# Kernel optimization log

Measured on AMD Instinct MI355X. Metric: run time of the kernel, lower is better.

Reference implementation:

```python
import jax, jax.numpy as jnp
import numpy as np

V = 50257      # vocab_size
EMB = 300      # emb_size
H = 512        # mcan_flat_out_size (GRU hidden)
HS = 256       # hidden_size (object proposal feature dim)
BH = 256       # bi_hidden_size (encoder output feature dim)
NP = 256       # num_proposal
ML = 50        # max_length (lang seq len)
AL = 20        # answer length -> 19 decode steps
NEG = -1e9


def setup_inputs() -> dict:
    key = jax.random.key(0)
    ks = jax.random.split(key, 30)
    s = 0.02
    n = lambda k, sh: (s * jax.random.normal(k, sh)).astype(jnp.float32)
    d = {}
    d["input_tok"] = jax.random.randint(ks[0], (1,), 0, V, dtype=jnp.int32)
    d["hidden"] = jax.random.normal(ks[1], (1, 1, H), jnp.float32)
    d["encoder_outputs"] = jax.random.normal(ks[2], (ML, BH), jnp.float32)
    d["object_proposals"] = jax.random.normal(ks[3], (NP, HS), jnp.float32)
    d["object_mask"] = jax.random.randint(ks[4], (1, NP), 0, 2, dtype=jnp.int32)
    d["lang_mask"] = jax.random.randint(ks[5], (1, ML), 0, 2, dtype=jnp.int32)
    d["answer_to_vocab"] = jax.random.randint(ks[6], (AL,), 0, V, dtype=jnp.int32)
    # learned params (dropout treated as eval/identity)
    d["emb"] = n(ks[7], (V, EMB))
    cin = H + EMB  # 812
    d["attn_w1"] = n(ks[8], (256, cin)); d["attn_b1"] = jnp.zeros((256,), jnp.float32)
    d["attn_w2"] = n(ks[9], (ML, 256)); d["attn_b2"] = jnp.zeros((ML,), jnp.float32)
    d["attn_op_w1"] = n(ks[10], (256, cin)); d["attn_op_b1"] = jnp.zeros((256,), jnp.float32)
    d["attn_op_w2"] = n(ks[11], (NP, 256)); d["attn_op_b2"] = jnp.zeros((NP,), jnp.float32)
    comb_in = HS + BH + EMB  # 812
    d["cmb_w1"] = n(ks[12], (512, comb_in)); d["cmb_b1"] = jnp.zeros((512,), jnp.float32)
    d["cmb_w2"] = n(ks[13], (H, 512)); d["cmb_b2"] = jnp.zeros((H,), jnp.float32)
    d["gru_w_ih"] = n(ks[14], (3 * H, H)); d["gru_w_hh"] = n(ks[15], (3 * H, H))
    d["gru_b_ih"] = jnp.zeros((3 * H,), jnp.float32); d["gru_b_hh"] = jnp.zeros((3 * H,), jnp.float32)
    d["out_w"] = n(ks[16], (V, H)); d["out_b"] = jnp.zeros((V,), jnp.float32)
    return d


def reference(input_tok, hidden, encoder_outputs, object_proposals, object_mask,
              lang_mask, answer_to_vocab, emb, attn_w1, attn_b1, attn_w2, attn_b2,
              attn_op_w1, attn_op_b1, attn_op_w2, attn_op_b2, cmb_w1, cmb_b1,
              cmb_w2, cmb_b2, gru_w_ih, gru_w_hh, gru_b_ih, gru_b_hh, out_w, out_b):
    obj_m = object_mask.astype(bool)   # [1, NP]
    lang_m = lang_mask.astype(bool)    # [1, ML]
    # teacher forcing: step i embeds answer_to_vocab[i] (step 0 uses input_tok)
    tokens = jnp.concatenate([input_tok, answer_to_vocab[1:-1]])  # [AL-1]

    def step(h, tok):
        # h: [1,1,H]
        x = jax.nn.relu(emb[tok])[None, :]                     # [1,EMB]
        cat = jnp.concatenate([x, h[0]], axis=1)               # [1, EMB+H]
        # object attention
        a_op = jax.nn.relu(cat @ attn_op_w1.T + attn_op_b1) @ attn_op_w2.T + attn_op_b2
        a_op = jax.nn.softmax(jnp.where(obj_m, NEG, a_op), axis=1)   # [1,NP]
        ctx_op = a_op @ object_proposals                       # [1,HS]
        # language attention
        a_l = jax.nn.relu(cat @ attn_w1.T + attn_b1) @ attn_w2.T + attn_b2
        a_l = jax.nn.softmax(jnp.where(lang_m, NEG, a_l), axis=1)    # [1,ML]
        ctx = a_l @ encoder_outputs                            # [1,BH]
        comb = jnp.concatenate([x, ctx, ctx_op], axis=1)       # [1, EMB+BH+HS]
        g = jax.nn.relu(jax.nn.relu(comb @ cmb_w1.T + cmb_b1) @ cmb_w2.T + cmb_b2)  # [1,H]
        # GRU cell (torch gate order: r, z, n)
        gi = g @ gru_w_ih.T + gru_b_ih
        gh = h[0] @ gru_w_hh.T + gru_b_hh
        i_r, i_z, i_n = jnp.split(gi, 3, axis=1)
        h_r, h_z, h_n = jnp.split(gh, 3, axis=1)
        r = jax.nn.sigmoid(i_r + h_r)
        z = jax.nn.sigmoid(i_z + h_z)
        nn_ = jnp.tanh(i_n + r * h_n)
        h_new = (1.0 - z) * nn_ + z * h[0]                     # [1,H]
        logits = h_new @ out_w.T + out_b                       # [1,V]
        return h_new[None], (logits, a_l, a_op)

    _, (logits, attn_w, attn_ob_w) = jax.lax.scan(step, hidden, tokens)
    # logits: [AL-1,1,V]; attn_w: [AL-1,1,ML]; attn_ob_w: [AL-1,1,NP]
    return logits, attn_w, attn_ob_w
```

## Files before the change

### kernel.cpp

```cpp
#include <hip/hip_runtime.h>
#include <math.h>

#define T_STEPS 19
#define V 50257
#define EMB 300
#define HDIM 512
#define NP 256
#define ML 50
#define CIN 812
#define NEGV -1e9f
#define NBLK 128

#define OFF_X      0
#define OFF_POP    5700
#define OFF_PL     10564
#define OFF_PC     15428
#define OFF_HS     25156
#define OFF_H1OP   35396
#define OFF_H1L    35652
#define OFF_C1     37444
#define OFF_G      37956
#define OFF_LOGOP  38468
#define OFF_LOGL   38724
#define OFF_MPROP  38788
#define OFF_MENC   169860
#define OFF_BAR    195460

#define OUT_LOGITS 0
#define OUT_ATTW   ((long)T_STEPS * V)
#define OUT_ATTOB  (OUT_ATTW + (long)T_STEPS * ML)

__device__ __forceinline__ float wred(float v) {
  v += __shfl_xor(v, 32, 64);
  v += __shfl_xor(v, 16, 64);
  v += __shfl_xor(v, 8, 64);
  v += __shfl_xor(v, 4, 64);
  v += __shfl_xor(v, 2, 64);
  v += __shfl_xor(v, 1, 64);
  return v;
}

__device__ __forceinline__ float dot4(float4 a, float4 b) {
  return a.x * b.x + a.y * b.y + a.z * b.z + a.w * b.w;
}

__device__ __forceinline__ void gstore(float* p, float v) {
  __hip_atomic_store(p, v, __ATOMIC_RELAXED, __HIP_MEMORY_SCOPE_AGENT);
}
__device__ __forceinline__ float ld1c(const float* p) {
  return __hip_atomic_load(p, __ATOMIC_RELAXED, __HIP_MEMORY_SCOPE_AGENT);
}
__device__ __forceinline__ float2 ld2c(const float* p) {
  unsigned long long u = __hip_atomic_load((const unsigned long long*)p,
                                           __ATOMIC_RELAXED, __HIP_MEMORY_SCOPE_AGENT);
  float2 r;
  r.x = __uint_as_float((unsigned)u);
  r.y = __uint_as_float((unsigned)(u >> 32));
  return r;
}
__device__ __forceinline__ float4 ld4c(const float* p) {
  float2 a = ld2c(p), b = ld2c(p + 2);
  return make_float4(a.x, a.y, b.x, b.y);
}

__device__ __forceinline__ void gbar(float* wsb, unsigned bar) {
  asm volatile("s_waitcnt vmcnt(0)" ::: "memory");
  __syncthreads();
  unsigned* base = (unsigned*)(wsb + OFF_BAR);
  if (threadIdx.x == 0) {
    __hip_atomic_store(base + 16 + 16 * blockIdx.x, bar, __ATOMIC_RELAXED, __HIP_MEMORY_SCOPE_AGENT);
  }
  if (blockIdx.x == 0 && threadIdx.x < 64) {
    unsigned* fa = base + 16 + 32 * threadIdx.x;
    unsigned* fb = fa + 16;
    while (__hip_atomic_load(fa, __ATOMIC_RELAXED, __HIP_MEMORY_SCOPE_AGENT) < bar ||
           __hip_atomic_load(fb, __ATOMIC_RELAXED, __HIP_MEMORY_SCOPE_AGENT) < bar) {
      __builtin_amdgcn_s_sleep(1);
    }
    if (threadIdx.x == 0) {
      __hip_atomic_store(base, bar, __ATOMIC_RELAXED, __HIP_MEMORY_SCOPE_AGENT);
    }
  } else if (threadIdx.x == 0) {
    while (__hip_atomic_load(base, __ATOMIC_RELAXED, __HIP_MEMORY_SCOPE_AGENT) < bar) {
      __builtin_amdgcn_s_sleep(1);
    }
  }
  __syncthreads();
}

__global__ void k_pre1(const int* __restrict__ tok0, const int* __restrict__ ans,
                       const float* __restrict__ emb, const float* __restrict__ hidden,
                       float* __restrict__ ws) {
  int tid = blockIdx.x * 256 + threadIdx.x;
  if (tid < T_STEPS * EMB) {
    int s = tid / EMB, j = tid - s * EMB;
    int t = (s == 0) ? tok0[0] : ans[s];
    float v = emb[(long)t * EMB + j];
    ws[OFF_X + tid] = v > 0.f ? v : 0.f;
  } else {
    int k = tid - T_STEPS * EMB;
    if (k < HDIM) ws[OFF_HS + k] = hidden[k];
  }
}

__global__ void k_pre2(const float* __restrict__ w1op, const float* __restrict__ b1op,
                       const float* __restrict__ w1l,  const float* __restrict__ b1l,
                       const float* __restrict__ wc1,  const float* __restrict__ bc1,
                       float* __restrict__ ws) {
  int gw = (blockIdx.x * 256 + threadIdx.x) >> 6;
  int lane = threadIdx.x & 63;
  int s = gw >> 10;
  int rr = gw & 1023;
  if (s >= T_STEPS) return;
  const float* wrow; const float* bias; float* dst; int r;
  if (rr < 256)      { r = rr;       wrow = w1op + (long)r * CIN; bias = b1op; dst = ws + OFF_POP + s * 256 + r; }
  else if (rr < 512) { r = rr - 256; wrow = w1l  + (long)r * CIN; bias = b1l;  dst = ws + OFF_PL  + s * 256 + r; }
  else               { r = rr - 512; wrow = wc1  + (long)r * CIN; bias = bc1;  dst = ws + OFF_PC  + s * 512 + r; }
  const float* x = ws + OFF_X + s * EMB;
  float acc = 0.f;
#pragma unroll
  for (int it = 0; it < 5; ++it) {
    int j = it * 64 + lane;
    if (j < EMB) acc += wrow[j] * x[j];
  }
  acc = wred(acc);
  if (lane == 0) *dst = acc + bias[r];
}

#define LDSF 12850
__global__ void __launch_bounds__(256) k_mprep(const float* __restrict__ cw1,
                                               const float* __restrict__ prop,
                                               const float* __restrict__ enc,
                                               float* __restrict__ ws) {
  __shared__ float lds[LDSF];
  int tid = threadIdx.x, r = blockIdx.x;
  float acc = 0.f;
  for (int kc = 0; kc < 8; ++kc) {
    __syncthreads();
#pragma unroll
    for (int i = 0; i < 8; ++i) {
      int f = tid + 256 * i; int row = f >> 3, q = f & 7;
      float4 v = *(const float4*)(prop + (long)row * 256 + kc * 32 + 4 * q);
      float* p = lds + row * 33 + 4 * q;
      p[0] = v.x; p[1] = v.y; p[2] = v.z; p[3] = v.w;
    }
    __syncthreads();
    const float* wbase = cw1 + (long)r * CIN + 556 + kc * 32;
    const float* pl = lds + tid * 33;
#pragma unroll
    for (int k4 = 0; k4 < 8; ++k4) {
      float4 w4 = *(const float4*)(wbase + 4 * k4);
      const float* pp = pl + 4 * k4;
      acc += w4.x * pp[0] + w4.y * pp[1] + w4.z * pp[2] + w4.w * pp[3];
    }
  }
  ws[OFF_MPROP + (long)r * 256 + tid] = acc;
  __syncthreads();
  for (int i = 0; i < 13; ++i) {
    int f = tid + 256 * i;
    if (f < 3200) {
      int row = f >> 6, q = f & 63;
      float4 v = *(const float4*)(enc + (long)row * 256 + 4 * q);
      float* p = lds + row * 257 + 4 * q;
      p[0] = v.x; p[1] = v.y; p[2] = v.z; p[3] = v.w;
    }
  }
  __syncthreads();
  if (tid < ML) {
    const float* wb2 = cw1 + (long)r * CIN + 300;
    const float* el = lds + tid * 257;
    float a2 = 0.f;
#pragma unroll 8
    for (int k = 0; k < 256; ++k) a2 += wb2[k] * el[k];
    ws[OFF_MENC + (long)r * ML + tid] = a2;
  }
}

__global__ void __launch_bounds__(256) k_recur(
    const float* __restrict__ w1op, const float* __restrict__ w1l,
    const float* __restrict__ whh,  const float* __restrict__ bhh,
    const float* __restrict__ w2op, const float* __restrict__ b2op,
    const float* __restrict__ w2l,  const float* __restrict__ b2l,
    const int* __restrict__ obj_mask, const int* __restrict__ lang_mask,
    const float* __restrict__ wc2,  const float* __restrict__ bc2,
    const float* __restrict__ wih,  const float* __restrict__ bih,
    float* ws, float* __restrict__ out) {
  const int tid = threadIdx.x;
  const int lane = tid & 63;
  const int wv = (blockIdx.x << 2) + (tid >> 6);
  unsigned bar = 1;
  __shared__ float red[256];
  __shared__ __align__(16) float sm_aop[256];
  __shared__ float sm_al[64];

  for (int s = 0; s < T_STEPS; ++s) {
    float gh_r, gh_z, gh_n;
    {
      const float* h = ws + OFF_HS + s * HDIM;
      float4 ha = ld4c(h + 4 * lane);
      float4 hb = ld4c(h + 256 + 4 * lane);
      const float* w0 = (wv < 256) ? (w1op + (long)wv * CIN + 300)
                                   : (w1l + (long)(wv - 256) * CIN + 300);
      const float* w1r = whh + (long)wv * HDIM;
      const float* w2r = whh + (long)(wv + 512) * HDIM;
      const float* w3r = whh + (long)(wv + 1024) * HDIM;
      float a0 = dot4(*(const float4*)(w0 + 4 * lane), ha) + dot4(*(const float4*)(w0 + 256 + 4 * lane), hb);
      float a1 = dot4(*(const float4*)(w1r + 4 * lane), ha) + dot4(*(const float4*)(w1r + 256 + 4 * lane), hb);
      float a2 = dot4(*(const float4*)(w2r + 4 * lane), ha) + dot4(*(const float4*)(w2r + 256 + 4 * lane), hb);
      float a3 = dot4(*(const float4*)(w3r + 4 * lane), ha) + dot4(*(const float4*)(w3r + 256 + 4 * lane), hb);
      a0 = wred(a0); a1 = wred(a1); a2 = wred(a2); a3 = wred(a3);
      gh_r = a1 + bhh[wv];
      gh_z = a2 + bhh[512 + wv];
      gh_n = a3 + bhh[1024 + wv];
      if (lane == 0) {
        if (wv < 256) {
          float v = a0 + ws[OFF_POP + s * 256 + wv];
          gstore(ws + OFF_H1OP + wv, v > 0.f ? v : 0.f);
        } else {
          float v = a0 + ws[OFF_PL + s * 256 + (wv - 256)];
          gstore(ws + OFF_H1L + (wv - 256), v > 0.f ? v : 0.f);
        }
      }
    }
    gbar(ws, bar++);
    if (wv < 306) {
      if (wv < 256) {
        float4 h1 = ld4c(ws + OFF_H1OP + 4 * lane);
        const float* wr = w2op + (long)wv * 256;
        float acc = wred(dot4(*(const float4*)(wr + 4 * lane), h1));
        if (lane == 0) gstore(ws + OFF_LOGOP + wv, acc + b2op[wv]);
      } else {
        int r = wv - 256;
        float4 h1 = ld4c(ws + OFF_H1L + 4 * lane);
        const float* wr = w2l + (long)r * 256;
        float acc = wred(dot4(*(const float4*)(wr + 4 * lane), h1));
        if (lane == 0) gstore(ws + OFF_LOGL + r, acc + b2l[r]);
      }
    }
    gbar(ws, bar++);
    {
      float lv = ld1c(ws + OFF_LOGOP + tid);
      float vo = (obj_mask[tid] != 0) ? NEGV : lv;
      red[tid] = vo; __syncthreads();
      for (int st = 128; st > 0; st >>= 1) { if (tid < st) red[tid] = fmaxf(red[tid], red[tid + st]); __syncthreads(); }
      float mo = red[0]; __syncthreads();
      float eo = expf(vo - mo);
      red[tid] = eo; __syncthreads();
      for (int st = 128; st > 0; st >>= 1) { if (tid < st) red[tid] += red[tid + st]; __syncthreads(); }
      float aop = eo / red[0];
      sm_aop[tid] = aop;
      __syncthreads();
      float ll = (tid < ML) ? ld1c(ws + OFF_LOGL + tid) : 0.f;
      float vl = (tid < ML) ? ((lang_mask[tid] != 0) ? NEGV : ll) : -3e38f;
      red[tid] = vl; __syncthreads();
      for (int st = 128; st > 0; st >>= 1) { if (tid < st) red[tid] = fmaxf(red[tid], red[tid + st]); __syncthreads(); }
      float ml_ = red[0]; __syncthreads();
      float el = (tid < ML) ? expf(vl - ml_) : 0.f;
      red[tid] = el; __syncthreads();
      for (int st = 128; st > 0; st >>= 1) { if (tid < st) red[tid] += red[tid + st]; __syncthreads(); }
      float al = el / red[0];
      if (tid < 64) sm_al[tid] = (tid < ML) ? al : 0.f;
      __syncthreads();
      if (blockIdx.x == 0) {
        out[OUT_ATTOB + (long)s * NP + tid] = aop;
        if (tid < ML) out[OUT_ATTW + (long)s * ML + tid] = al;
      }
      int r = wv;
      const float* mp = ws + OFF_MPROP + (long)r * 256;
      float4 m4 = *(const float4*)(mp + 4 * lane);
      float4 a4 = *(const float4*)(&sm_aop[4 * lane]);
      float acc = dot4(m4, a4);
      if (lane < ML) acc += ws[OFF_MENC + (long)r * ML + lane] * sm_al[lane];
      acc = wred(acc);
      if (lane == 0) {
        float v = acc + ws[OFF_PC + s * HDIM + r];
        gstore(ws + OFF_C1 + r, v > 0.f ? v : 0.f);
      }
    }
    gbar(ws, bar++);
    {
      int r = wv;
      float4 ca = ld4c(ws + OFF_C1 + 4 * lane);
      float4 cb = ld4c(ws + OFF_C1 + 256 + 4 * lane);
      const float* wr = wc2 + (long)r * HDIM;
      float acc = wred(dot4(*(const float4*)(wr + 4 * lane), ca) + dot4(*(const float4*)(wr + 256 + 4 * lane), cb));
      if (lane == 0) {
        float v = acc + bc2[r];
        gstore(ws + OFF_G + r, v > 0.f ? v : 0.f);
      }
    }
    gbar(ws, bar++);
    {
      int j = wv;
      float4 ga = ld4c(ws + OFF_G + 4 * lane);
      float4 gb = ld4c(ws + OFF_G + 256 + 4 * lane);
      const float* p0 = wih + (long)j * HDIM;
      const float* p1 = wih + (long)(j + 512) * HDIM;
      const float* p2 = wih + (long)(j + 1024) * HDIM;
      float a0 = dot4(*(const float4*)(p0 + 4 * lane), ga) + dot4(*(const float4*)(p0 + 256 + 4 * lane), gb);
      float a1 = dot4(*(const float4*)(p1 + 4 * lane), ga) + dot4(*(const float4*)(p1 + 256 + 4 * lane), gb);
      float a2 = dot4(*(const float4*)(p2 + 4 * lane), ga) + dot4(*(const float4*)(p2 + 256 + 4 * lane), gb);
      a0 = wred(a0); a1 = wred(a1); a2 = wred(a2);
      if (lane == 0) {
        float ir = a0 + bih[j], iz = a1 + bih[512 + j], in_ = a2 + bih[1024 + j];
        float rg = 1.f / (1.f + expf(-(ir + gh_r)));
        float zg = 1.f / (1.f + expf(-(iz + gh_z)));
        float ng = tanhf(in_ + rg * gh_n);
        float hp = ld1c(ws + OFF_HS + s * HDIM + j);
        gstore(ws + OFF_HS + (s + 1) * HDIM + j, (1.f - zg) * ng + zg * hp);
      }
    }
    gbar(ws, bar++);
  }
}

__global__ void __launch_bounds__(256) k_final2(const float* __restrict__ ow,
                                                const float* __restrict__ ob,
                                                const float* __restrict__ ws,
                                                float* __restrict__ out) {
  __shared__ __align__(16) float wl[256 * 36];
  __shared__ __align__(16) float hl[T_STEPS * 512];
  int tid = threadIdx.x;
  long rbase = (long)blockIdx.x * 256;
  for (int i = tid; i < T_STEPS * 512; i += 256) hl[i] = ws[OFF_HS + 512 + i];
  float4 st[8];
#pragma unroll
  for (int i = 0; i < 8; ++i) {
    int f = tid + 256 * i; int row = f >> 3, q = f & 7;
    long r = rbase + row;
    st[i] = (r < V) ? *(const float4*)(ow + r * 512 + 4 * q) : make_float4(0.f, 0.f, 0.f, 0.f);
  }
  float acc[T_STEPS];
#pragma unroll
  for (int s = 0; s < T_STEPS; ++s) acc[s] = 0.f;
  __syncthreads();
  for (int c = 0; c < 16; ++c) {
#pragma unroll
    for (int i = 0; i < 8; ++i) {
      int f = tid + 256 * i; int row = f >> 3, q = f & 7;
      float* p = wl + row * 36 + 4 * q;
      p[0] = st[i].x; p[1] = st[i].y; p[2] = st[i].z; p[3] = st[i].w;
    }
    __syncthreads();
    if (c < 15) {
#pragma unroll
      for (int i = 0; i < 8; ++i) {
        int f = tid + 256 * i; int row = f >> 3, q = f & 7;
        long r = rbase + row;
        st[i] = (r < V) ? *(const float4*)(ow + r * 512 + (c + 1) * 32 + 4 * q) : make_float4(0.f, 0.f, 0.f, 0.f);
      }
    }
    const float* wp = wl + tid * 36;
#pragma unroll
    for (int kq = 0; kq < 8; ++kq) {
      float4 w4 = *(const float4*)(wp + 4 * kq);
      const float* hb = hl + c * 32 + 4 * kq;
#pragma unroll
      for (int s = 0; s < T_STEPS; ++s) {
        float4 h4 = *(const float4*)(hb + s * 512);
        acc[s] += dot4(w4, h4);
      }
    }
    __syncthreads();
  }
  long r = rbase + tid;
  if (r < V) {
    float b = ob[r];
#pragma unroll
    for (int s = 0; s < T_STEPS; ++s) out[OUT_LOGITS + (long)s * V + r] = acc[s] + b;
  }
}

extern "C" void kernel_launch(void* const* d_in, const int* in_sizes, int n_in,
                              void* d_out, int out_size, void* d_ws, size_t ws_size,
                              hipStream_t stream) {
  const int*   input_tok  = (const int*)d_in[0];
  const float* hidden     = (const float*)d_in[1];
  const float* enc        = (const float*)d_in[2];
  const float* prop       = (const float*)d_in[3];
  const int*   obj_mask   = (const int*)d_in[4];
  const int*   lang_mask  = (const int*)d_in[5];
  const int*   ans        = (const int*)d_in[6];
  const float* emb        = (const float*)d_in[7];
  const float* attn_w1    = (const float*)d_in[8];
  const float* attn_b1    = (const float*)d_in[9];
  const float* attn_w2    = (const float*)d_in[10];
  const float* attn_b2    = (const float*)d_in[11];
  const float* attn_op_w1 = (const float*)d_in[12];
  const float* attn_op_b1 = (const float*)d_in[13];
  const float* attn_op_w2 = (const float*)d_in[14];
  const float* attn_op_b2 = (const float*)d_in[15];
  const float* cmb_w1     = (const float*)d_in[16];
  const float* cmb_b1     = (const float*)d_in[17];
  const float* cmb_w2     = (const float*)d_in[18];
  const float* cmb_b2     = (const float*)d_in[19];
  const float* gw_ih      = (const float*)d_in[20];
  const float* gw_hh      = (const float*)d_in[21];
  const float* gb_ih      = (const float*)d_in[22];
  const float* gb_hh      = (const float*)d_in[23];
  const float* out_w      = (const float*)d_in[24];
  const float* out_b      = (const float*)d_in[25];
  float* out = (float*)d_out;
  float* ws  = (float*)d_ws;

  hipMemsetAsync((char*)d_ws + (size_t)OFF_BAR * 4, 0, 8448, stream);
  k_pre1<<<25, 256, 0, stream>>>(input_tok, ans, emb, hidden, ws);
  k_pre2<<<4864, 256, 0, stream>>>(attn_op_w1, attn_op_b1, attn_w1, attn_b1, cmb_w1, cmb_b1, ws);
  k_mprep<<<512, 256, 0, stream>>>(cmb_w1, prop, enc, ws);
  k_recur<<<NBLK, 256, 0, stream>>>(attn_op_w1, attn_w1, gw_hh, gb_hh,
                                    attn_op_w2, attn_op_b2, attn_w2, attn_b2,
                                    obj_mask, lang_mask, cmb_w2, cmb_b2,
                                    gw_ih, gb_ih, ws, out);
  k_final2<<<(V + 255) / 256, 256, 0, stream>>>(out_w, out_b, ws, out);
}
```

Before: 459.7 us.

## Halve recurrent grid to 64 blocks, two rows per wave, flat barrier

The persistent recurrent kernel now runs on 64 blocks instead of 128, and each wave computes two output rows per stage instead of one. The grid barrier drops the master-block gather-and-broadcast and has every block poll all 64 flags directly, which removes one hop of latency per barrier. This targets the cost of the five grid barriers per decode step. In exchange, each wave does twice the dot-product work per stage and each block issues more flag polls.

```diff
diff --git a/kernel.cpp b/kernel.cpp
--- a/kernel.cpp
+++ b/kernel.cpp
@@ -9,7 +9,7 @@
 #define ML 50
 #define CIN 812
 #define NEGV -1e9f
-#define NBLK 128
+#define NBLK 64
 
 #define OFF_X      0
 #define OFF_POP    5700
@@ -66,22 +66,14 @@
 __device__ __forceinline__ void gbar(float* wsb, unsigned bar) {
   asm volatile("s_waitcnt vmcnt(0)" ::: "memory");
   __syncthreads();
-  unsigned* base = (unsigned*)(wsb + OFF_BAR);
+  unsigned* flags = (unsigned*)(wsb + OFF_BAR) + 16;
   if (threadIdx.x == 0) {
-    __hip_atomic_store(base + 16 + 16 * blockIdx.x, bar, __ATOMIC_RELAXED, __HIP_MEMORY_SCOPE_AGENT);
-  }
-  if (blockIdx.x == 0 && threadIdx.x < 64) {
-    unsigned* fa = base + 16 + 32 * threadIdx.x;
-    unsigned* fb = fa + 16;
-    while (__hip_atomic_load(fa, __ATOMIC_RELAXED, __HIP_MEMORY_SCOPE_AGENT) < bar ||
-           __hip_atomic_load(fb, __ATOMIC_RELAXED, __HIP_MEMORY_SCOPE_AGENT) < bar) {
-      __builtin_amdgcn_s_sleep(1);
-    }
-    if (threadIdx.x == 0) {
-      __hip_atomic_store(base, bar, __ATOMIC_RELAXED, __HIP_MEMORY_SCOPE_AGENT);
-    }
-  } else if (threadIdx.x == 0) {
-    while (__hip_atomic_load(base, __ATOMIC_RELAXED, __HIP_MEMORY_SCOPE_AGENT) < bar) {
+    __hip_atomic_store(flags + 16 * blockIdx.x, bar, __ATOMIC_RELAXED, __HIP_MEMORY_SCOPE_AGENT);
+  }
+  asm volatile("" ::: "memory");
+  if (threadIdx.x < 64) {
+    unsigned* f = flags + 16 * threadIdx.x;
+    while (__hip_atomic_load(f, __ATOMIC_RELAXED, __HIP_MEMORY_SCOPE_AGENT) < bar) {
       __builtin_amdgcn_s_sleep(1);
     }
   }
@@ -188,53 +180,59 @@
   const int tid = threadIdx.x;
   const int lane = tid & 63;
   const int wv = (blockIdx.x << 2) + (tid >> 6);
+  const int r0 = 2 * wv, r1 = 2 * wv + 1;
   unsigned bar = 1;
   __shared__ float red[256];
   __shared__ __align__(16) float sm_aop[256];
   __shared__ float sm_al[64];
 
   for (int s = 0; s < T_STEPS; ++s) {
-    float gh_r, gh_z, gh_n;
+    float ghr0, ghz0, ghn0, ghr1, ghz1, ghn1;
     {
       const float* h = ws + OFF_HS + s * HDIM;
       float4 ha = ld4c(h + 4 * lane);
       float4 hb = ld4c(h + 256 + 4 * lane);
-      const float* w0 = (wv < 256) ? (w1op + (long)wv * CIN + 300)
-                                   : (w1l + (long)(wv - 256) * CIN + 300);
-      const float* w1r = whh + (long)wv * HDIM;
-      const float* w2r = whh + (long)(wv + 512) * HDIM;
-      const float* w3r = whh + (long)(wv + 1024) * HDIM;
-      float a0 = dot4(*(const float4*)(w0 + 4 * lane), ha) + dot4(*(const float4*)(w0 + 256 + 4 * lane), hb);
-      float a1 = dot4(*(const float4*)(w1r + 4 * lane), ha) + dot4(*(const float4*)(w1r + 256 + 4 * lane), hb);
-      float a2 = dot4(*(const float4*)(w2r + 4 * lane), ha) + dot4(*(const float4*)(w2r + 256 + 4 * lane), hb);
-      float a3 = dot4(*(const float4*)(w3r + 4 * lane), ha) + dot4(*(const float4*)(w3r + 256 + 4 * lane), hb);
-      a0 = wred(a0); a1 = wred(a1); a2 = wred(a2); a3 = wred(a3);
-      gh_r = a1 + bhh[wv];
-      gh_z = a2 + bhh[512 + wv];
-      gh_n = a3 + bhh[1024 + wv];
+      const float* wa0 = (r0 < 256) ? (w1op + (long)r0 * CIN + 300) : (w1l + (long)(r0 - 256) * CIN + 300);
+      const float* wa1 = (r1 < 256) ? (w1op + (long)r1 * CIN + 300) : (w1l + (long)(r1 - 256) * CIN + 300);
+      float a0 = dot4(*(const float4*)(wa0 + 4 * lane), ha) + dot4(*(const float4*)(wa0 + 256 + 4 * lane), hb);
+      float a1 = dot4(*(const float4*)(wa1 + 4 * lane), ha) + dot4(*(const float4*)(wa1 + 256 + 4 * lane), hb);
+      const float* p0 = whh + (long)r0 * HDIM;
+      const float* p1 = whh + (long)(r0 + 512) * HDIM;
+      const float* p2 = whh + (long)(r0 + 1024) * HDIM;
+      const float* p3 = whh + (long)r1 * HDIM;
+      const float* p4 = whh + (long)(r1 + 512) * HDIM;
+      const float* p5 = whh + (long)(r1 + 1024) * HDIM;
+      float b0 = dot4(*(const float4*)(p0 + 4 * lane), ha) + dot4(*(const float4*)(p0 + 256 + 4 * lane), hb);
+      float b1 = dot4(*(const float4*)(p1 + 4 * lane), ha) + dot4(*(const float4*)(p1 + 256 + 4 * lane), hb);
+      float b2 = dot4(*(const float4*)(p2 + 4 * lane), ha) + dot4(*(const float4*)(p2 + 256 + 4 * lane), hb);
+      float b3 = dot4(*(const float4*)(p3 + 4 * lane), ha) + dot4(*(const float4*)(p3 + 256 + 4 * lane), hb);
+      float b4 = dot4(*(const float4*)(p4 + 4 * lane), ha) + dot4(*(const float4*)(p4 + 256 + 4 * lane), hb);
+      float b5 = dot4(*(const float4*)(p5 + 4 * lane), ha) + dot4(*(const float4*)(p5 + 256 + 4 * lane), hb);
+      a0 = wred(a0); a1 = wred(a1);
+      b0 = wred(b0); b1 = wred(b1); b2 = wred(b2);
+      b3 = wred(b3); b4 = wred(b4); b5 = wred(b5);
+      ghr0 = b0 + bhh[r0]; ghz0 = b1 + bhh[512 + r0]; ghn0 = b2 + bhh[1024 + r0];
+      ghr1 = b3 + bhh[r1]; ghz1 = b4 + bhh[512 + r1]; ghn1 = b5 + bhh[1024 + r1];
       if (lane == 0) {
-        if (wv < 256) {
-          float v = a0 + ws[OFF_POP + s * 256 + wv];
-          gstore(ws + OFF_H1OP + wv, v > 0.f ? v : 0.f);
-        } else {
-          float v = a0 + ws[OFF_PL + s * 256 + (wv - 256)];
-          gstore(ws + OFF_H1L + (wv - 256), v > 0.f ? v : 0.f);
-        }
+        float v0 = a0 + ((r0 < 256) ? ws[OFF_POP + s * 256 + r0] : ws[OFF_PL + s * 256 + (r0 - 256)]);
+        float v1 = a1 + ((r1 < 256) ? ws[OFF_POP + s * 256 + r1] : ws[OFF_PL + s * 256 + (r1 - 256)]);
+        float* d0 = (r0 < 256) ? (ws + OFF_H1OP + r0) : (ws + OFF_H1L + (r0 - 256));
+        float* d1 = (r1 < 256) ? (ws + OFF_H1OP + r1) : (ws + OFF_H1L + (r1 - 256));
+        gstore(d0, v0 > 0.f ? v0 : 0.f);
+        gstore(d1, v1 > 0.f ? v1 : 0.f);
       }
     }
     gbar(ws, bar++);
-    if (wv < 306) {
-      if (wv < 256) {
-        float4 h1 = ld4c(ws + OFF_H1OP + 4 * lane);
-        const float* wr = w2op + (long)wv * 256;
-        float acc = wred(dot4(*(const float4*)(wr + 4 * lane), h1));
-        if (lane == 0) gstore(ws + OFF_LOGOP + wv, acc + b2op[wv]);
-      } else {
-        int r = wv - 256;
-        float4 h1 = ld4c(ws + OFF_H1L + 4 * lane);
-        const float* wr = w2l + (long)r * 256;
-        float acc = wred(dot4(*(const float4*)(wr + 4 * lane), h1));
-        if (lane == 0) gstore(ws + OFF_LOGL + r, acc + b2l[r]);
+    {
+      float4 h1 = ld4c(ws + OFF_H1OP + 4 * lane);
+      const float* wr = w2op + (long)wv * 256;
+      float acc = wred(dot4(*(const float4*)(wr + 4 * lane), h1));
+      if (lane == 0) gstore(ws + OFF_LOGOP + wv, acc + b2op[wv]);
+      if (wv < ML) {
+        float4 h1l = ld4c(ws + OFF_H1L + 4 * lane);
+        const float* wrl = w2l + (long)wv * 256;
+        float accl = wred(dot4(*(const float4*)(wrl + 4 * lane), h1l));
+        if (lane == 0) gstore(ws + OFF_LOGL + wv, accl + b2l[wv]);
       }
     }
     gbar(ws, bar++);
@@ -265,49 +263,71 @@
         out[OUT_ATTOB + (long)s * NP + tid] = aop;
         if (tid < ML) out[OUT_ATTW + (long)s * ML + tid] = al;
       }
-      int r = wv;
-      const float* mp = ws + OFF_MPROP + (long)r * 256;
-      float4 m4 = *(const float4*)(mp + 4 * lane);
       float4 a4 = *(const float4*)(&sm_aop[4 * lane]);
-      float acc = dot4(m4, a4);
-      if (lane < ML) acc += ws[OFF_MENC + (long)r * ML + lane] * sm_al[lane];
-      acc = wred(acc);
+      const float* mp0 = ws + OFF_MPROP + (long)r0 * 256;
+      const float* mp1 = ws + OFF_MPROP + (long)r1 * 256;
+      float acc0 = dot4(*(const float4*)(mp0 + 4 * lane), a4);
+      float acc1 = dot4(*(const float4*)(mp1 + 4 * lane), a4);
+      if (lane < ML) {
+        float alv = sm_al[lane];
+        acc0 += ws[OFF_MENC + (long)r0 * ML + lane] * alv;
+        acc1 += ws[OFF_MENC + (long)r1 * ML + lane] * alv;
+      }
+      acc0 = wred(acc0); acc1 = wred(acc1);
       if (lane == 0) {
-        float v = acc + ws[OFF_PC + s * HDIM + r];
-        gstore(ws + OFF_C1 + r, v > 0.f ? v : 0.f);
+        float v0 = acc0 + ws[OFF_PC + s * HDIM + r0];
+        float v1 = acc1 + ws[OFF_PC + s * HDIM + r1];
+        gstore(ws + OFF_C1 + r0, v0 > 0.f ? v0 : 0.f);
+        gstore(ws + OFF_C1 + r1, v1 > 0.f ? v1 : 0.f);
       }
     }
     gbar(ws, bar++);
     {
-      int r = wv;
       float4 ca = ld4c(ws + OFF_C1 + 4 * lane);
       float4 cb = ld4c(ws + OFF_C1 + 256 + 4 * lane);
-      const float* wr = wc2 + (long)r * HDIM;
-      float acc = wred(dot4(*(const float4*)(wr + 4 * lane), ca) + dot4(*(const float4*)(wr + 256 + 4 * lane), cb));
+      const float* q0 = wc2 + (long)r0 * HDIM;
+      const float* q1 = wc2 + (long)r1 * HDIM;
+      float acc0 = dot4(*(const float4*)(q0 + 4 * lane), ca) + dot4(*(const float4*)(q0 + 256 + 4 * lane), cb);
+      float acc1 = dot4(*(const float4*)(q1 + 4 * lane), ca) + dot4(*(const float4*)(q1 + 256 + 4 * lane), cb);
+      acc0 = wred(acc0); acc1 = wred(acc1);
       if (lane == 0) {
-        float v = acc + bc2[r];
-        gstore(ws + OFF_G + r, v > 0.f ? v : 0.f);
+        float v0 = acc0 + bc2[r0];
+        float v1 = acc1 + bc2[r1];
+        gstore(ws + OFF_G + r0, v0 > 0.f ? v0 : 0.f);
+        gstore(ws + OFF_G + r1, v1 > 0.f ? v1 : 0.f);
       }
     }
     gbar(ws, bar++);
     {
-      int j = wv;
       float4 ga = ld4c(ws + OFF_G + 4 * lane);
       float4 gb = ld4c(ws + OFF_G + 256 + 4 * lane);
-      const float* p0 = wih + (long)j * HDIM;
-      const float* p1 = wih + (long)(j + 512) * HDIM;
-      const float* p2 = wih + (long)(j + 1024) * HDIM;
+      const float* p0 = wih + (long)r0 * HDIM;
+      const float* p1 = wih + (long)(r0 + 512) * HDIM;
+      const float* p2 = wih + (long)(r0 + 1024) * HDIM;
+      const float* p3 = wih + (long)r1 * HDIM;
+      const float* p4 = wih + (long)(r1 + 512) * HDIM;
+      const float* p5 = wih + (long)(r1 + 1024) * HDIM;
       float a0 = dot4(*(const float4*)(p0 + 4 * lane), ga) + dot4(*(const float4*)(p0 + 256 + 4 * lane), gb);
       float a1 = dot4(*(const float4*)(p1 + 4 * lane), ga) + dot4(*(const float4*)(p1 + 256 + 4 * lane), gb);
       float a2 = dot4(*(const float4*)(p2 + 4 * lane), ga) + dot4(*(const float4*)(p2 + 256 + 4 * lane), gb);
+      float a3 = dot4(*(const float4*)(p3 + 4 * lane), ga) + dot4(*(const float4*)(p3 + 256 + 4 * lane), gb);
+      float a4_ = dot4(*(const float4*)(p4 + 4 * lane), ga) + dot4(*(const float4*)(p4 + 256 + 4 * lane), gb);
+      float a5 = dot4(*(const float4*)(p5 + 4 * lane), ga) + dot4(*(const float4*)(p5 + 256 + 4 * lane), gb);
       a0 = wred(a0); a1 = wred(a1); a2 = wred(a2);
+      a3 = wred(a3); a4_ = wred(a4_); a5 = wred(a5);
       if (lane == 0) {
-        float ir = a0 + bih[j], iz = a1 + bih[512 + j], in_ = a2 + bih[1024 + j];
-        float rg = 1.f / (1.f + expf(-(ir + gh_r)));
-        float zg = 1.f / (1.f + expf(-(iz + gh_z)));
-        float ng = tanhf(in_ + rg * gh_n);
-        float hp = ld1c(ws + OFF_HS + s * HDIM + j);
-        gstore(ws + OFF_HS + (s + 1) * HDIM + j, (1.f - zg) * ng + zg * hp);
+        float ir0 = a0 + bih[r0], iz0 = a1 + bih[512 + r0], in0 = a2 + bih[1024 + r0];
+        float rg0 = 1.f / (1.f + expf(-(ir0 + ghr0)));
+        float zg0 = 1.f / (1.f + expf(-(iz0 + ghz0)));
+        float ng0 = tanhf(in0 + rg0 * ghn0);
+        float hp0 = ld1c(ws + OFF_HS + s * HDIM + r0);
+        gstore(ws + OFF_HS + (s + 1) * HDIM + r0, (1.f - zg0) * ng0 + zg0 * hp0);
+        float ir1 = a3 + bih[r1], iz1 = a4_ + bih[512 + r1], in1 = a5 + bih[1024 + r1];
+        float rg1 = 1.f / (1.f + expf(-(ir1 + ghr1)));
+        float zg1 = 1.f / (1.f + expf(-(iz1 + ghz1)));
+        float ng1 = tanhf(in1 + rg1 * ghn1);
+        float hp1 = ld1c(ws + OFF_HS + s * HDIM + r1);
+        gstore(ws + OFF_HS + (s + 1) * HDIM + r1, (1.f - zg1) * ng1 + zg1 * hp1);
       }
     }
     gbar(ws, bar++);
```

New measurement: 419.2 us. 8.8% less time.
